# Optimization experiments

Measured on AMD Instinct MI355X. Metric: run time of the kernel, lower is better.

Reference implementation:

```python
import jax, jax.numpy as jnp
import numpy as np

TEMP = 0.1
LP_WEIGHT = 0.1
DIM = 128
N = 200000
E = 100000
POS_LEN = 2048
EDGE_POS_LEN = 4096
POS_CAP = 8192  # pos_prob = edge_prob[nonzero][:8192] in the original


def setup_inputs() -> dict:
    key = jax.random.key(0)
    k1, k2, k3 = jax.random.split(key, 3)
    feat_all = jax.random.normal(k1, (N, DIM), dtype=jnp.float32)
    q = jax.random.normal(k2, (DIM,), dtype=jnp.float32)
    edge_prob = jax.random.normal(k3, (E,), dtype=jnp.float32)
    # positives occupy the first pos_len / edge_pos_len entries (torch.split semantics)
    labels = jnp.concatenate([jnp.ones((POS_LEN,), jnp.int64), jnp.zeros((N - POS_LEN,), jnp.int64)])
    edge_labels = jnp.concatenate([jnp.ones((EDGE_POS_LEN,), jnp.int64), jnp.zeros((E - EDGE_POS_LEN,), jnp.int64)])
    return {
        "feat_all": feat_all,
        "q": q,
        "edge_prob": edge_prob,
        "edge_labels": edge_labels,
        "adj_mat": jnp.zeros((1, 1), jnp.float32),
        "batch_item": jnp.zeros((1,), jnp.float32),
        "labels": labels,
        "raw_feat_all": jnp.zeros((1, DIM), jnp.float32),
        "raw_centroid": jnp.zeros((DIM,), jnp.float32),
        "pos_len": POS_LEN,
        "edge_pos_len": EDGE_POS_LEN,
    }


def _ce_pos_vs_shared_negs(pos, neg, temp):
    # CrossEntropy(cat([pos_i, negs]) / temp, label=0), mean over i.
    # Equivalent to logsumexp over [pos_i, negs] minus pos_i, computed
    # WITHOUT materializing the [P, Z+1] repeated-negative matrix:
    # the negatives' logsumexp is shared across all rows.
    inv_t = 1.0 / temp
    lse_neg = jax.nn.logsumexp(neg * inv_t)  # scalar, shared by every row
    return jnp.mean(jnp.logaddexp(pos * inv_t, lse_neg) - pos * inv_t)


def reference(feat_all, q, edge_prob, edge_labels, adj_mat, batch_item, labels,
              raw_feat_all, raw_centroid, pos_len, edge_pos_len):
    eps = 1e-12  # F.normalize eps clamp
    qn = q / jnp.maximum(jnp.linalg.norm(q), eps)                                   # [D]
    fn = feat_all / jnp.maximum(jnp.linalg.norm(feat_all, axis=1, keepdims=True), eps)  # [N, D]
    q2all = fn @ qn  # [N] cosine scores

    # contrastive loss: each positive vs ALL (shared) negatives
    contras_loss = _ce_pos_vs_shared_negs(q2all[:pos_len], q2all[pos_len:], TEMP)

    # link-prediction loss (is_lp=True): positive edges (capped at 8192) vs shared negative edges
    pe = min(edge_pos_len, POS_CAP)
    lp_loss = _ce_pos_vs_shared_negs(edge_prob[:pe], edge_prob[edge_pos_len:], TEMP)

    outlier_loss = contras_loss + LP_WEIGHT * lp_loss
    scores = q2all  # second mm(feat_all, q) is identical to q2all
    return outlier_loss, scores, contras_loss, lp_loss
```

## Files before the change

kernel.cpp:

```cpp
#include <hip/hip_runtime.h>
#include <math.h>

#define DIMD    128
#define POSLEN  2048
#define EDGEPOS 4096
#define NBLK    2048
#define NGRP    (NBLK * 16)
#define FTH     1024

typedef float vfloat4 __attribute__((ext_vector_type(4)));

#define NTL4(p) __builtin_nontemporal_load((const vfloat4*)(p))

__device__ __forceinline__ double wave_reduce_add_d(double v) {
    #pragma unroll
    for (int m = 32; m >= 1; m >>= 1) v += __shfl_xor(v, m, 64);
    return v;
}

__global__ __launch_bounds__(256) void k_main(
        const float* __restrict__ feat, const float* __restrict__ q,
        const float* __restrict__ ep, int nrows, int nedge,
        float* __restrict__ scores_out,
        double* __restrict__ part_s, double* __restrict__ part_e) {
    __shared__ double sh[4], she[4];
    const int tid  = threadIdx.x;
    const int lane = tid & 63;
    const int wv   = tid >> 6;
    const int b    = blockIdx.x;

    const int nedge4 = nedge >> 2;
    const float* pbase = ep + EDGEPOS;
    double eacc = 0.0;
    for (int i = b * 256 + tid; i < nedge4; i += NBLK * 256) {
        vfloat4 v = NTL4(pbase + 4 * (size_t)i);
        eacc += (double)__expf(10.0f * v.x) + (double)__expf(10.0f * v.y)
              + (double)__expf(10.0f * v.z) + (double)__expf(10.0f * v.w);
    }
    if (b == 0 && tid == 0)
        for (int i = nedge4 << 2; i < nedge; ++i)
            eacc += (double)__expf(10.0f * ep[EDGEPOS + i]);

    const int sl  = lane & 15;
    const int grp = lane >> 4;
    const float4* q4 = (const float4*)q;
    const float4 qa = q4[sl];
    const float4 qb = q4[16 + sl];
    float qn2 = qa.x*qa.x + qa.y*qa.y + qa.z*qa.z + qa.w*qa.w
              + qb.x*qb.x + qb.y*qb.y + qb.z*qb.z + qb.w*qb.w;
    #pragma unroll
    for (int m = 8; m >= 1; m >>= 1) qn2 += __shfl_xor(qn2, m, 64);
    const float invq = 1.0f / fmaxf(sqrtf(qn2), 1e-12f);

    const int g0 = b * 16 + wv * 4 + grp;
    float facc = 0.0f;
    vfloat4 fa, fb;
    if (g0 < nrows) {
        const float* row = feat + (size_t)g0 * DIMD;
        fa = NTL4(row + 4 * sl); fb = NTL4(row + 64 + 4 * sl);
    }
    for (int r = g0; r < nrows; r += NGRP) {
        const vfloat4 ca = fa, cb = fb;
        const int rn = r + NGRP;
        if (rn < nrows) {
            const float* nx = feat + (size_t)rn * DIMD;
            fa = NTL4(nx + 4 * sl); fb = NTL4(nx + 64 + 4 * sl);
        }
        float dot = ca.x*qa.x + ca.y*qa.y + ca.z*qa.z + ca.w*qa.w
                  + cb.x*qb.x + cb.y*qb.y + cb.z*qb.z + cb.w*qb.w;
        float n2  = ca.x*ca.x + ca.y*ca.y + ca.z*ca.z + ca.w*ca.w
                  + cb.x*cb.x + cb.y*cb.y + cb.z*cb.z + cb.w*cb.w;
        #pragma unroll
        for (int m = 8; m >= 1; m >>= 1) {
            dot += __shfl_xor(dot, m, 64);
            n2  += __shfl_xor(n2, m, 64);
        }
        if (sl == 0) {
            float s = dot * (1.0f / fmaxf(sqrtf(n2), 1e-12f)) * invq;
            scores_out[r] = s;
            if (r >= POSLEN) facc += __expf(10.0f * s - 10.0f);
        }
    }
    double acc  = wave_reduce_add_d((double)facc);
    double acce = wave_reduce_add_d(eacc);
    if (lane == 0) { sh[wv] = acc; she[wv] = acce; }
    __syncthreads();
    if (tid == 0) {
        part_s[b] = sh[0] + sh[1] + sh[2] + sh[3];
        part_e[b] = she[0] + she[1] + she[2] + she[3];
    }
}

__global__ __launch_bounds__(1024) void k3_final(
        const float* __restrict__ scores, const float* __restrict__ ep,
        const double* __restrict__ part_s, const double* __restrict__ part_e,
        float* __restrict__ out0, float* __restrict__ out_c, float* __restrict__ out_lp) {
    __shared__ double sh0[16], sh1[16];
    const int tid  = threadIdx.x;
    const int lane = tid & 63;
    const int wv   = tid >> 6;

    double p0 = 0.0, p1 = 0.0;
    for (int i = tid; i < NBLK; i += FTH) { p0 += part_s[i]; p1 += part_e[i]; }
    p0 = wave_reduce_add_d(p0);
    p1 = wave_reduce_add_d(p1);
    if (lane == 0) { sh0[wv] = p0; sh1[wv] = p1; }
    __syncthreads();
    double w0 = 0.0, w1 = 0.0;
    #pragma unroll
    for (int i = 0; i < 16; ++i) { w0 += sh0[i]; w1 += sh1[i]; }
    const float lse_s = (float)(10.0 + log(w0));
    const float lse_e = (float)log(w1);
    __syncthreads();

    double a1 = 0.0, a2 = 0.0;
    for (int i = tid; i < POSLEN; i += FTH) {
        float p = scores[i] * 10.0f;
        float m = fmaxf(p, lse_s);
        a1 += (double)(m - p + log1pf(__expf(fminf(p, lse_s) - m)));
    }
    for (int i = tid; i < EDGEPOS; i += FTH) {
        float p = ep[i] * 10.0f;
        float m = fmaxf(p, lse_e);
        a2 += (double)(m - p + log1pf(__expf(fminf(p, lse_e) - m)));
    }
    a1 = wave_reduce_add_d(a1);
    a2 = wave_reduce_add_d(a2);
    if (lane == 0) { sh0[wv] = a1; sh1[wv] = a2; }
    __syncthreads();
    if (tid == 0) {
        double c = 0.0, l = 0.0;
        #pragma unroll
        for (int i = 0; i < 16; ++i) { c += sh0[i]; l += sh1[i]; }
        c /= (double)POSLEN;
        l /= (double)EDGEPOS;
        *out0   = (float)(c + 0.1 * l);
        *out_c  = (float)c;
        *out_lp = (float)l;
    }
}

extern "C" void kernel_launch(void* const* d_in, const int* in_sizes, int n_in,
                              void* d_out, int out_size, void* d_ws, size_t ws_size,
                              hipStream_t stream) {
    const float* feat = (const float*)d_in[0];
    const float* q    = (const float*)d_in[1];
    const float* ep   = (const float*)d_in[2];
    const int N = in_sizes[0] / DIMD;
    const int E = in_sizes[2];

    float* out      = (float*)d_out;
    double* part_s  = (double*)d_ws;
    double* part_e  = part_s + NBLK;

    hipLaunchKernelGGL(k_main, dim3(NBLK), dim3(256), 0, stream,
                       feat, q, ep, N, E - EDGEPOS, out + 1, part_s, part_e);
    hipLaunchKernelGGL(k3_final, dim3(1), dim3(FTH), 0, stream,
                       out + 1, ep, part_s, part_e, out, out + 1 + N, out + 2 + N);
}
```

Before: 170.5 us.

## Remap lanes to contiguous row halves and double-depth prefetch feature rows

Each wave now covers four rows with 32 lanes per row, each lane loading one contiguous 512-byte float4 span instead of two split 256-byte pieces. Loads are prefetched two iterations ahead to keep more memory requests in flight, and scores are written with nontemporal stores. Row indices are clamped so tail loads stay in range. The cost is more live registers, twice the shuffle reductions per row, and redundant clamped loads at the tail.

```diff
diff --git a/kernel.cpp b/kernel.cpp
--- a/kernel.cpp
+++ b/kernel.cpp
@@ -5,7 +5,7 @@
 #define POSLEN  2048
 #define EDGEPOS 4096
 #define NBLK    2048
-#define NGRP    (NBLK * 16)
+#define SROWS   (NBLK * 16)
 #define FTH     1024
 
 typedef float vfloat4 __attribute__((ext_vector_type(4)));
@@ -41,44 +41,57 @@
         for (int i = nedge4 << 2; i < nedge; ++i)
             eacc += (double)__expf(10.0f * ep[EDGEPOS + i]);
 
-    const int sl  = lane & 15;
-    const int grp = lane >> 4;
+    const int sub  = lane & 31;
+    const int half = lane >> 5;
     const float4* q4 = (const float4*)q;
-    const float4 qa = q4[sl];
-    const float4 qb = q4[16 + sl];
-    float qn2 = qa.x*qa.x + qa.y*qa.y + qa.z*qa.z + qa.w*qa.w
-              + qb.x*qb.x + qb.y*qb.y + qb.z*qb.z + qb.w*qb.w;
+    const float4 qv = q4[sub];
+    float qn2 = qv.x*qv.x + qv.y*qv.y + qv.z*qv.z + qv.w*qv.w;
     #pragma unroll
-    for (int m = 8; m >= 1; m >>= 1) qn2 += __shfl_xor(qn2, m, 64);
+    for (int m = 16; m >= 1; m >>= 1) qn2 += __shfl_xor(qn2, m, 64);
     const float invq = 1.0f / fmaxf(sqrtf(qn2), 1e-12f);
 
-    const int g0 = b * 16 + wv * 4 + grp;
+    const int g0      = b * 16 + wv * 4;
+    const int laneoff = 4 * sub;
+
+    auto addrA = [&](int r) { int ra = r + half;     ra = ra < nrows ? ra : nrows - 1;
+                              return feat + (size_t)ra * DIMD + laneoff; };
+    auto addrB = [&](int r) { int rb = r + 2 + half; rb = rb < nrows ? rb : nrows - 1;
+                              return feat + (size_t)rb * DIMD + laneoff; };
+
+    vfloat4 a0 = {0,0,0,0}, b0 = {0,0,0,0}, a1 = {0,0,0,0}, b1 = {0,0,0,0};
+    if (g0 < nrows)         { a0 = NTL4(addrA(g0));         b0 = NTL4(addrB(g0)); }
+    if (g0 + SROWS < nrows) { a1 = NTL4(addrA(g0 + SROWS)); b1 = NTL4(addrB(g0 + SROWS)); }
+
     float facc = 0.0f;
-    vfloat4 fa, fb;
-    if (g0 < nrows) {
-        const float* row = feat + (size_t)g0 * DIMD;
-        fa = NTL4(row + 4 * sl); fb = NTL4(row + 64 + 4 * sl);
-    }
-    for (int r = g0; r < nrows; r += NGRP) {
-        const vfloat4 ca = fa, cb = fb;
-        const int rn = r + NGRP;
-        if (rn < nrows) {
-            const float* nx = feat + (size_t)rn * DIMD;
-            fa = NTL4(nx + 4 * sl); fb = NTL4(nx + 64 + 4 * sl);
+    for (int r = g0; r < nrows; r += SROWS) {
+        const vfloat4 ca = a0, cb = b0;
+        a0 = a1; b0 = b1;
+        const int rn = r + 2 * SROWS;
+        if (rn < nrows) { a1 = NTL4(addrA(rn)); b1 = NTL4(addrB(rn)); }
+
+        float da = ca.x*qv.x + ca.y*qv.y + ca.z*qv.z + ca.w*qv.w;
+        float na = ca.x*ca.x + ca.y*ca.y + ca.z*ca.z + ca.w*ca.w;
+        float db = cb.x*qv.x + cb.y*qv.y + cb.z*qv.z + cb.w*qv.w;
+        float nb = cb.x*cb.x + cb.y*cb.y + cb.z*cb.z + cb.w*cb.w;
+        #pragma unroll
+        for (int m = 16; m >= 1; m >>= 1) {
+            da += __shfl_xor(da, m, 64);
+            na += __shfl_xor(na, m, 64);
+            db += __shfl_xor(db, m, 64);
+            nb += __shfl_xor(nb, m, 64);
         }
-        float dot = ca.x*qa.x + ca.y*qa.y + ca.z*qa.z + ca.w*qa.w
-                  + cb.x*qb.x + cb.y*qb.y + cb.z*qb.z + cb.w*qb.w;
-        float n2  = ca.x*ca.x + ca.y*ca.y + ca.z*ca.z + ca.w*ca.w
-                  + cb.x*cb.x + cb.y*cb.y + cb.z*cb.z + cb.w*cb.w;
-        #pragma unroll
-        for (int m = 8; m >= 1; m >>= 1) {
-            dot += __shfl_xor(dot, m, 64);
-            n2  += __shfl_xor(n2, m, 64);
-        }
-        if (sl == 0) {
-            float s = dot * (1.0f / fmaxf(sqrtf(n2), 1e-12f)) * invq;
-            scores_out[r] = s;
-            if (r >= POSLEN) facc += __expf(10.0f * s - 10.0f);
+        if (sub == 0) {
+            const int ra = r + half, rb = r + 2 + half;
+            if (ra < nrows) {
+                float s = da * (1.0f / fmaxf(sqrtf(na), 1e-12f)) * invq;
+                __builtin_nontemporal_store(s, scores_out + ra);
+                if (ra >= POSLEN) facc += __expf(10.0f * s - 10.0f);
+            }
+            if (rb < nrows) {
+                float s = db * (1.0f / fmaxf(sqrtf(nb), 1e-12f)) * invq;
+                __builtin_nontemporal_store(s, scores_out + rb);
+                if (rb >= POSLEN) facc += __expf(10.0f * s - 10.0f);
+            }
         }
     }
     double acc  = wave_reduce_add_d((double)facc);
```

Result: slower. 174.9 us (+2.6%).
